# Kernel tuning notes

Hardware: AMD Instinct MI355X
Metric: run time of the kernel (lower is better)

## Reference

```python
import jax, jax.numpy as jnp
import numpy as np

H = 384  # LSTM hidden size


def _conv1d(x, w, b, stride):
    # x: [B, T, Cin], w: [K, Cin, Cout] (flax 'SAME' padding, channels-last)
    y = jax.lax.conv_general_dilated(
        x, w, window_strides=(stride,), padding='SAME',
        dimension_numbers=('NWC', 'WIO', 'NWC'))
    return y + b


def _lstm(x, Wi, Wh, b, reverse):
    # x: [B, T, D]; Wi: [D, 4H] (input proj, no bias in flax LSTMCell input dense),
    # Wh: [H, 4H] (recurrent proj), b: [4H]. Gate order: i, f, g, o.
    if reverse:
        x = x[:, ::-1]
    B = x.shape[0]
    # precompute all input-to-gate projections in one big GEMM: [B, T, 4H]
    xg = jnp.einsum('btd,dh->bth', x, Wi)

    def step(carry, xg_t):
        c, h = carry
        z = xg_t + h @ Wh + b                      # [B, 4H]
        i, f, g, o = jnp.split(z, 4, axis=-1)
        i = jax.nn.sigmoid(i)
        f = jax.nn.sigmoid(f)
        g = jnp.tanh(g)
        o = jax.nn.sigmoid(o)
        c = f * c + i * g
        h = o * jnp.tanh(c)
        return (c, h), h

    init = (jnp.zeros((B, H), x.dtype), jnp.zeros((B, H), x.dtype))
    _, hs = jax.lax.scan(step, init, jnp.swapaxes(xg, 0, 1))  # hs: [T, B, H]
    hs = jnp.swapaxes(hs, 0, 1)
    if reverse:  # keep_order=True: flip output back to original time order
        hs = hs[:, ::-1]
    return hs


def setup_inputs() -> dict:
    key = jax.random.key(0)
    ks = jax.random.split(key, 12)
    s = 0.05
    B, T = 128, 8000
    return {
        'x': jax.random.normal(ks[0], (B, T, 1), jnp.float32),
        'conv1_w': jax.random.normal(ks[1], (5, 1, 4), jnp.float32) * s,
        'conv1_b': jnp.zeros((4,), jnp.float32),
        'conv2_w': jax.random.normal(ks[2], (5, 4, 16), jnp.float32) * s,
        'conv2_b': jnp.zeros((16,), jnp.float32),
        'conv3_w': jax.random.normal(ks[3], (19, 16, H), jnp.float32) * s,
        'conv3_b': jnp.zeros((H,), jnp.float32),
        'lstm_Wi': jax.random.normal(ks[4], (5, H, 4 * H), jnp.float32) * s,
        'lstm_Wh': jax.random.normal(ks[5], (5, H, 4 * H), jnp.float32) * s,
        'lstm_b': jnp.zeros((5, 4 * H), jnp.float32),
        'dense_w': jax.random.normal(ks[6], (H, 5), jnp.float32) * s,
        'dense_b': jnp.zeros((5,), jnp.float32),
    }


def reference(x, conv1_w, conv1_b, conv2_w, conv2_b, conv3_w, conv3_b,
              lstm_Wi, lstm_Wh, lstm_b, dense_w, dense_b):
    # CNN feature extractor
    x = jax.nn.silu(_conv1d(x, conv1_w, conv1_b, 1))
    x = jax.nn.silu(_conv1d(x, conv2_w, conv2_b, 1))
    x = jax.nn.silu(_conv1d(x, conv3_w, conv3_b, 5))   # [B, T/5, 384]
    # 5 stacked LSTMs, layers 1,3,5 reversed (keep_order), layers 2,4 forward
    for i in range(5):
        x = _lstm(x, lstm_Wi[i], lstm_Wh[i], lstm_b[i], reverse=(i % 2 == 0))
    # CTC head
    return x @ dense_w + dense_b                       # [B, T/5, 5]
```

## Files before the change

kernel.cpp:

```cpp
#include <hip/hip_runtime.h>
#include <math.h>

#define B_SZ 128
#define T_IN 8000
#define T_OUT 1600
#define HDIM 384
#define GDIM 1536
#define TC 40
#define NCHUNK (T_OUT / TC)
#define NTILES (12 * (B_SZ * TC / 128))
#define NLB 64

typedef _Float16 f16;
typedef __attribute__((ext_vector_type(2))) _Float16 f16x2;
typedef __attribute__((ext_vector_type(4))) _Float16 f16x4;
typedef __attribute__((ext_vector_type(8))) _Float16 f16x8;
typedef __attribute__((ext_vector_type(4))) float f32x4;
typedef __attribute__((ext_vector_type(4))) unsigned int u32x4;

__device__ inline float fdot2(f16x2 a, f16x2 b, float c) {
#if __has_builtin(__builtin_amdgcn_fdot2)
  return __builtin_amdgcn_fdot2(a, b, c, false);
#else
  return fmaf((float)a[0], (float)b[0], fmaf((float)a[1], (float)b[1], c));
#endif
}

__device__ inline float rcp_fast(float x) {
#if __has_builtin(__builtin_amdgcn_rcpf)
  return __builtin_amdgcn_rcpf(x);
#else
  return 1.f / x;
#endif
}
__device__ inline float sigf(float z) { return rcp_fast(1.f + __expf(-z)); }
__device__ inline float tanh_fast(float z) {
  z = fminf(fmaxf(z, -15.f), 15.f);
  float e = __expf(2.f * z);
  return (e - 1.f) * rcp_fast(e + 1.f);
}

__global__ __launch_bounds__(256) void conv12_kernel(
    const float* __restrict__ x, const float* __restrict__ w1, const float* __restrict__ b1,
    const float* __restrict__ w2, const float* __restrict__ b2, f16* __restrict__ y2) {
  __shared__ float sw1[20], sb1[4], sw2[320], sb2[16];
  int tid = threadIdx.x;
  if (tid < 20) sw1[tid] = w1[tid];
  if (tid < 4)  sb1[tid] = b1[tid];
  if (tid < 16) sb2[tid] = b2[tid];
  for (int i = tid; i < 320; i += 256) sw2[i] = w2[i];
  __syncthreads();
  int flat = blockIdx.x * 256 + tid;
  int b = flat / T_IN, t = flat % T_IN;
  const float* xb = x + (size_t)b * T_IN;
  float xv[9];
#pragma unroll
  for (int d = 0; d < 9; ++d) {
    int tt = t + d - 4;
    xv[d] = (tt >= 0 && tt < T_IN) ? xb[tt] : 0.f;
  }
  float y1[5][4];
#pragma unroll
  for (int u = 0; u < 5; ++u) {
    int tau = t + u - 2;
    bool valid = (tau >= 0 && tau < T_IN);
#pragma unroll
    for (int co = 0; co < 4; ++co) {
      float a = sb1[co];
#pragma unroll
      for (int k = 0; k < 5; ++k) a = fmaf(xv[u + k], sw1[k * 4 + co], a);
      y1[u][co] = valid ? (a / (1.f + expf(-a))) : 0.f;
    }
  }
  f16x8 o0, o1;
#pragma unroll
  for (int co = 0; co < 16; ++co) {
    float a = sb2[co];
#pragma unroll
    for (int u = 0; u < 5; ++u)
#pragma unroll
      for (int ci = 0; ci < 4; ++ci)
        a = fmaf(y1[u][ci], sw2[(u * 4 + ci) * 16 + co], a);
    float sv = a / (1.f + expf(-a));
    if (co < 8) o0[co] = (f16)sv; else o1[co - 8] = (f16)sv;
  }
  f16x8* dst = (f16x8*)(y2 + (size_t)flat * 16);
  dst[0] = o0;
  dst[1] = o1;
}

__global__ __launch_bounds__(256) void w3cvt_kernel(
    const float* __restrict__ w3, f16* __restrict__ w3t) {
  int idx = blockIdx.x * 256 + threadIdx.x;
  int c = idx / 320, k = idx - c * 320;
  w3t[idx] = (k < 304) ? (f16)w3[(size_t)k * 384 + c] : (f16)0.f;
}

#define C3M 32
#define C3K 320
#define INSP 24
#define BSTP 40

__global__ __launch_bounds__(384) void conv3_kernel(
    const f16* __restrict__ y2, const f16* __restrict__ w3t,
    const float* __restrict__ b3, f16* __restrict__ act) {
  __shared__ f16 in_s[176 * INSP];
  __shared__ f16 bs_t[384 * BSTP];
  int tid = threadIdx.x;
  int b = blockIdx.y;
  int t0 = blockIdx.x * C3M;
  int base_t = t0 * 5 - 7;
  for (int j = tid; j < 352; j += 384) {
    int tau = j >> 1, ci0 = (j & 1) * 8;
    int tt = base_t + tau;
    f16x8 v = {};
    if (tt >= 0 && tt < T_IN)
      v = *(const f16x8*)(y2 + ((size_t)b * T_IN + tt) * 16 + ci0);
    *(f16x8*)&in_s[tau * INSP + ci0] = v;
  }
  int wv = tid >> 6;
  int l = tid & 63;
  int lm = l & 15;
  int lk = l >> 4;
  f32x4 acc[2][4];
#pragma unroll
  for (int mt = 0; mt < 2; ++mt)
#pragma unroll
    for (int q = 0; q < 4; ++q) acc[mt][q] = (f32x4){0.f, 0.f, 0.f, 0.f};
  for (int ks = 0; ks < 10; ++ks) {
    __syncthreads();
    for (int u = tid; u < 1536; u += 384) {
      int c = u >> 2, k8 = u & 3;
      *(f16x8*)&bs_t[c * BSTP + k8 * 8] =
          *(const f16x8*)(w3t + (size_t)c * C3K + ks * 32 + k8 * 8);
    }
    __syncthreads();
    int kg = ks * 32 + lk * 8;
    int kk = kg >> 4, ci = kg & 15;
    f16x8 a0 = *(const f16x8*)&in_s[(lm * 5 + kk) * INSP + ci];
    f16x8 a1 = *(const f16x8*)&in_s[((lm + 16) * 5 + kk) * INSP + ci];
#pragma unroll
    for (int q = 0; q < 4; ++q) {
      f16x8 bf = *(const f16x8*)&bs_t[((wv * 4 + q) * 16 + lm) * BSTP + lk * 8];
      acc[0][q] = __builtin_amdgcn_mfma_f32_16x16x32_f16(a0, bf, acc[0][q], 0, 0, 0);
      acc[1][q] = __builtin_amdgcn_mfma_f32_16x16x32_f16(a1, bf, acc[1][q], 0, 0, 0);
    }
  }
#pragma unroll
  for (int mt = 0; mt < 2; ++mt)
#pragma unroll
    for (int q = 0; q < 4; ++q) {
      int n = (wv * 4 + q) * 16 + lm;
      float bv = b3[n];
#pragma unroll
      for (int r = 0; r < 4; ++r) {
        int m = mt * 16 + lk * 4 + r;
        float a = acc[mt][q][r] + bv;
        a = a / (1.f + expf(-a));
        act[((size_t)b * T_OUT + t0 + m) * HDIM + n] = (f16)a;
      }
    }
}

__global__ __launch_bounds__(256) void whcvt_kernel(
    const float* __restrict__ Wh, f16x2* __restrict__ whB) {
  size_t idx = (size_t)blockIdx.x * 256 + threadIdx.x;
  int d = (int)(idx & 3);
  size_t r1 = idx >> 2;
  int lane = (int)(r1 & 63);
  size_t r2 = r1 >> 6;
  int ks = (int)(r2 % 12);
  size_t r3 = r2 / 12;
  int nt = (int)(r3 % 12);
  size_t r4 = r3 / 12;
  int isl = (int)(r4 & 7);
  int L = (int)(r4 >> 3);
  int cz = nt * 16 + (lane & 15);
  int gate = cz & 3;
  int jj = cz >> 2;
  int gcol = gate * 384 + isl * 48 + jj;
  int k2d = ks * 16 + (lane >> 4) * 4 + d;
  const float* src = Wh + ((size_t)L * 384 + 2 * k2d) * 1536 + gcol;
  f16x2 v;
  v[0] = (f16)src[0];
  v[1] = (f16)src[1536];
  whB[idx] = v;
}

__global__ __launch_bounds__(256) void gemm_xg_kernel(
    const f16* __restrict__ act, const float* __restrict__ Bw,
    f16* __restrict__ C, int lo) {
  __shared__ f16x2 As2[8 * 136];
  __shared__ f16x2 Bs2[8 * 128];
  int tid = threadIdx.x;
  int n0 = blockIdx.x * 128;
  int m0 = blockIdx.y * 128;
  int am = tid >> 2;
  int ak = (tid & 3) * 4;
  int bk = tid >> 5;
  int bn = (tid & 31) * 4;
  int row0 = m0 + am, row1 = row0 + 64;
  const f16* Ap0 = act + ((size_t)(row0 / TC) * T_OUT + lo + row0 % TC) * HDIM + ak;
  const f16* Ap1 = act + ((size_t)(row1 / TC) * T_OUT + lo + row1 % TC) * HDIM + ak;
  const float* Bp = Bw + (size_t)(2 * bk) * GDIM + n0 + bn;
  f16x4 ra0 = *(const f16x4*)Ap0;
  f16x4 ra1 = *(const f16x4*)Ap1;
  float4 rb0 = *(const float4*)Bp;
  float4 rb1 = *(const float4*)(Bp + (size_t)GDIM);
  float acc[8][8];
#pragma unroll
  for (int i = 0; i < 8; ++i)
#pragma unroll
    for (int j = 0; j < 8; ++j) acc[i][j] = 0.f;
  int tx = tid & 15, ty = tid >> 4;
  for (int kt = 0; kt < 24; ++kt) {
    int ak2 = ak >> 1;
    As2[(ak2 + 0) * 136 + am] = (f16x2){ra0[0], ra0[1]};
    As2[(ak2 + 1) * 136 + am] = (f16x2){ra0[2], ra0[3]};
    As2[(ak2 + 0) * 136 + am + 64] = (f16x2){ra1[0], ra1[1]};
    As2[(ak2 + 1) * 136 + am + 64] = (f16x2){ra1[2], ra1[3]};
    Bs2[bk * 128 + bn + 0] = (f16x2){(f16)rb0.x, (f16)rb1.x};
    Bs2[bk * 128 + bn + 1] = (f16x2){(f16)rb0.y, (f16)rb1.y};
    Bs2[bk * 128 + bn + 2] = (f16x2){(f16)rb0.z, (f16)rb1.z};
    Bs2[bk * 128 + bn + 3] = (f16x2){(f16)rb0.w, (f16)rb1.w};
    __syncthreads();
    if (kt < 23) {
      Ap0 += 16; Ap1 += 16; Bp += (size_t)16 * GDIM;
      ra0 = *(const f16x4*)Ap0;
      ra1 = *(const f16x4*)Ap1;
      rb0 = *(const float4*)Bp;
      rb1 = *(const float4*)(Bp + (size_t)GDIM);
    }
#pragma unroll
    for (int k2 = 0; k2 < 8; ++k2) {
      f16x8 a0 = *(const f16x8*)&As2[k2 * 136 + ty * 4];
      f16x8 a1 = *(const f16x8*)&As2[k2 * 136 + 64 + ty * 4];
      f16x8 b0 = *(const f16x8*)&Bs2[k2 * 128 + tx * 4];
      f16x8 b1 = *(const f16x8*)&Bs2[k2 * 128 + 64 + tx * 4];
      f16x2 av[8], bv[8];
#pragma unroll
      for (int q = 0; q < 4; ++q) {
        av[q] = (f16x2){a0[2 * q], a0[2 * q + 1]};
        av[q + 4] = (f16x2){a1[2 * q], a1[2 * q + 1]};
        bv[q] = (f16x2){b0[2 * q], b0[2 * q + 1]};
        bv[q + 4] = (f16x2){b1[2 * q], b1[2 * q + 1]};
      }
#pragma unroll
      for (int i = 0; i < 8; ++i)
#pragma unroll
        for (int j = 0; j < 8; ++j) acc[i][j] = fdot2(av[i], bv[j], acc[i][j]);
    }
    __syncthreads();
  }
#pragma unroll
  for (int i = 0; i < 8; ++i) {
    int mi = (i < 4) ? (ty * 4 + i) : (64 + ty * 4 + i - 4);
    f16* Cp = C + (size_t)(m0 + mi) * GDIM + n0;
    f16x4 p0, p1;
    p0[0] = (f16)acc[i][0]; p0[1] = (f16)acc[i][1]; p0[2] = (f16)acc[i][2]; p0[3] = (f16)acc[i][3];
    p1[0] = (f16)acc[i][4]; p1[1] = (f16)acc[i][5]; p1[2] = (f16)acc[i][6]; p1[3] = (f16)acc[i][7];
    *(f16x4*)(Cp + tx * 4) = p0;
    *(f16x4*)(Cp + 64 + tx * 4) = p1;
  }
}

#define HSTR 784

union FusedSh {
  struct { char h2s[16 * HSTR]; unsigned pub[16 * 25]; } L;
  struct { f16x2 As2[3][8 * 136]; f16x2 Bs2[3][8 * 128]; } G;
  char pad[25600];
};

__global__ __launch_bounds__(768, 1) void fused_kernel(
    const f16* __restrict__ xgc_rd, f16* __restrict__ xgc_wr,
    const f16* __restrict__ whB, const float* __restrict__ bias,
    f16* __restrict__ act, float* __restrict__ cst, const float* __restrict__ Wi,
    unsigned* __restrict__ xh,
    int lo_l, int lo_g, int reverse, int first, int do_gemm, int epoch) {
  __shared__ FusedSh sh;
  int tid = threadIdx.x;

  if (blockIdx.x < NLB) {
    int wid = blockIdx.x;
    int g = wid & 7;
    int isl = wid >> 3;
    int b0 = g * 16;
    int nt = tid >> 6;
    int l = tid & 63;
    int bg = l >> 4;
    int qj = (l >> 2) & 3;
    int gate = l & 3;
    int jj = nt * 4 + qj;
    int hcol = isl * 48 + jj;
    int gcol = gate * 384 + isl * 48 + jj;

    f16x8 wreg[12];
    {
      const f16x8* wp = (const f16x8*)whB + (size_t)(isl * 12 + nt) * 12 * 64 + l;
#pragma unroll
      for (int ks = 0; ks < 12; ++ks) wreg[ks] = wp[(size_t)ks * 64];
#pragma unroll
      for (int ks = 0; ks < 12; ++ks) asm volatile("" : "+v"(wreg[ks]));
    }
    float bias_own = bias[gcol];

    float c_reg[4];
    if (first) {
#pragma unroll
      for (int r = 0; r < 4; ++r) c_reg[r] = 0.f;
      for (int i = tid; i < 16 * HSTR / 16; i += 768)
        *(f16x8*)(sh.L.h2s + i * 16) = (f16x8){};
    } else {
      int tprev = reverse ? (lo_l + TC) : (lo_l - 1);
#pragma unroll
      for (int r = 0; r < 4; ++r)
        c_reg[r] = cst[(size_t)(b0 + bg * 4 + r) * HDIM + hcol];
      int flat = tid * 8;
      int bt = flat / 384, c0 = flat % 384;
      *(f16x8*)(sh.L.h2s + bt * HSTR + c0 * 2) =
          *(const f16x8*)(act + ((size_t)(b0 + bt) * T_OUT + tprev) * HDIM + c0);
    }
    __syncthreads();

    const char* arow = sh.L.h2s + (l & 15) * HSTR + (l >> 4) * 16;
    unsigned short* pubh = (unsigned short*)sh.L.pub;

    int k2 = (tid % 3 == 0) ? (768 + tid / 3) : -1;

    float xv[4];
    {
      int tl0 = reverse ? (TC - 1) : 0;
      const f16* xb = xgc_rd + ((size_t)(b0 + bg * 4) * TC + tl0) * GDIM + gcol;
#pragma unroll
      for (int r = 0; r < 4; ++r) xv[r] = (float)xb[(size_t)r * TC * GDIM];
    }

    for (int s = 0; s < TC; ++s) {
      int t = reverse ? (lo_l + TC - 1 - s) : (lo_l + s);

      f32x4 acc = {0.f, 0.f, 0.f, 0.f};
#pragma unroll
      for (int ks = 0; ks < 12; ++ks) {
        f16x8 a = *(const f16x8*)(arow + ks * 64);
        acc = __builtin_amdgcn_mfma_f32_16x16x32_f16(a, wreg[ks], acc, 0, 0, 0);
      }

      f16 h16[4];
#pragma unroll
      for (int r = 0; r < 4; ++r) {
        float a = acc[r] + xv[r] + bias_own;
        float b = __shfl_xor(a, 1);
        float cc = __shfl_xor(a, 2);
        float dd = __shfl_xor(b, 2);
        float zi = (gate == 0) ? a : (gate == 1) ? b : (gate == 2) ? cc : dd;
        float zf = (gate == 1) ? a : (gate == 0) ? b : (gate == 3) ? cc : dd;
        float zg = (gate == 2) ? a : (gate == 3) ? b : (gate == 0) ? cc : dd;
        float zo = (gate == 3) ? a : (gate == 2) ? b : (gate == 1) ? cc : dd;
        float ig = sigf(zi), fg = sigf(zf), gv = tanh_fast(zg), og = sigf(zo);
        c_reg[r] = fg * c_reg[r] + ig * gv;
        h16[r] = (f16)(og * tanh_fast(c_reg[r]));
      }

      if (s + 1 < TC) {
        unsigned tag = (unsigned)(epoch * TC + s + 1);
        unsigned* slotbase = xh + (size_t)(s & 1) * 128 * 256;

        if (gate == 0) {
          int lcol = nt * 4 + qj;
#pragma unroll
          for (int r = 0; r < 4; ++r)
            pubh[(bg * 4 + r) * 50 + lcol] = __builtin_bit_cast(unsigned short, h16[r]);
        }
        __syncthreads();

        if (tid < 128) {
          int bt = tid >> 3, u = tid & 7;
          const unsigned* pw = sh.L.pub + bt * 25 + u * 3;
          u32x4 dnew;
          dnew[0] = pw[0]; dnew[1] = pw[1]; dnew[2] = pw[2]; dnew[3] = tag;
          u32x4* dp = (u32x4*)(slotbase + (((size_t)(b0 + bt) * 64) + isl * 8 + u) * 4);
          asm volatile("global_store_dwordx4 %0, %1, off sc0 sc1"
                       :: "v"(dp), "v"(dnew) : "memory");
        }

        if (gate == 0) {
#pragma unroll
          for (int r = 0; r < 4; ++r)
            act[((size_t)(b0 + bg * 4 + r) * T_OUT + t) * HDIM + hcol] = h16[r];
        }
        {
          int tl_n = reverse ? (TC - 2 - s) : (s + 1);
          const f16* xb = xgc_rd + ((size_t)(b0 + bg * 4) * TC + tl_n) * GDIM + gcol;
#pragma unroll
          for (int r = 0; r < 4; ++r) xv[r] = (float)xb[(size_t)r * TC * GDIM];
        }

        const u32x4* upA = nullptr; const u32x4* upB = nullptr;
        unsigned* dstA = nullptr; unsigned* dstB = nullptr;
#pragma unroll
        for (int uu = 0; uu < 2; ++uu) {
          int k = (uu == 0) ? tid : k2;
          if (uu == 1 && k < 0) break;
          int bt = k >> 6, rem = k & 63;
          int isl_src = rem >> 3, u = rem & 7;
          unsigned* dst = (unsigned*)(sh.L.h2s + bt * HSTR + isl_src * 96 + u * 12);
          if (isl_src == isl) {
            const unsigned* pw = sh.L.pub + bt * 25 + u * 3;
            dst[0] = pw[0]; dst[1] = pw[1]; dst[2] = pw[2];
          } else {
            const u32x4* up = (const u32x4*)(slotbase + (((size_t)(b0 + bt) * 64) + rem) * 4);
            if (!upA) { upA = up; dstA = dst; } else { upB = up; dstB = dst; }
          }
        }
        if (upA && !upB) {
          u32x4 v;
          while (true) {
            asm volatile("global_load_dwordx4 %0, %1, off sc0 sc1\n\ts_waitcnt vmcnt(0)"
                         : "=v"(v) : "v"(upA) : "memory");
            if (v[3] >= tag) break;
            __builtin_amdgcn_s_sleep(1);
          }
          dstA[0] = v[0]; dstA[1] = v[1]; dstA[2] = v[2];
        } else if (upA && upB) {
          u32x4 v0, v1;
          while (true) {
            asm volatile("global_load_dwordx4 %0, %2, off sc0 sc1\n\t"
                         "global_load_dwordx4 %1, %3, off sc0 sc1\n\t"
                         "s_waitcnt vmcnt(0)"
                         : "=&v"(v0), "=&v"(v1) : "v"(upA), "v"(upB) : "memory");
            if (v0[3] >= tag && v1[3] >= tag) break;
            __builtin_amdgcn_s_sleep(1);
          }
          dstA[0] = v0[0]; dstA[1] = v0[1]; dstA[2] = v0[2];
          dstB[0] = v1[0]; dstB[1] = v1[1]; dstB[2] = v1[2];
        }
        __syncthreads();
      } else {
        if (gate == 0) {
#pragma unroll
          for (int r = 0; r < 4; ++r)
            act[((size_t)(b0 + bg * 4 + r) * T_OUT + t) * HDIM + hcol] = h16[r];
        }
      }
    }
    if (gate == 0) {
#pragma unroll
      for (int r = 0; r < 4; ++r)
        cst[(size_t)(b0 + bg * 4 + r) * HDIM + hcol] = c_reg[r];
    }
  } else {
    if (!do_gemm) return;
    int wid = blockIdx.x - NLB;
    int sub = tid >> 8;
    int stid = tid & 255;
    int tileid = wid + 192 * sub;
    bool valid = (tileid < NTILES);
    int tclamp = valid ? tileid : 0;
    int n0 = (tclamp % 12) * 128;
    int m0 = (tclamp / 12) * 128;
    f16x2* As2 = &sh.G.As2[sub][0];
    f16x2* Bs2 = &sh.G.Bs2[sub][0];
    int am = stid >> 2;
    int ak = (stid & 3) * 4;
    int bk = stid >> 5;
    int bn = (stid & 31) * 4;
    int row0 = m0 + am, row1 = row0 + 64;
    const f16* Ap0 = act + ((size_t)(row0 / TC) * T_OUT + lo_g + row0 % TC) * HDIM + ak;
    const f16* Ap1 = act + ((size_t)(row1 / TC) * T_OUT + lo_g + row1 % TC) * HDIM + ak;
    const float* Bp = Wi + (size_t)(2 * bk) * GDIM + n0 + bn;
    f16x4 ra0 = {}, ra1 = {};
    float4 rb0 = {}, rb1 = {};
    if (valid) {
      ra0 = *(const f16x4*)Ap0;
      ra1 = *(const f16x4*)Ap1;
      rb0 = *(const float4*)Bp;
      rb1 = *(const float4*)(Bp + (size_t)GDIM);
    }
    float acc[8][8];
#pragma unroll
    for (int i = 0; i < 8; ++i)
#pragma unroll
      for (int j = 0; j < 8; ++j) acc[i][j] = 0.f;
    int tx = stid & 15, ty = stid >> 4;
    for (int kt = 0; kt < 24; ++kt) {
      if (valid) {
        int ak2 = ak >> 1;
        As2[(ak2 + 0) * 136 + am] = (f16x2){ra0[0], ra0[1]};
        As2[(ak2 + 1) * 136 + am] = (f16x2){ra0[2], ra0[3]};
        As2[(ak2 + 0) * 136 + am + 64] = (f16x2){ra1[0], ra1[1]};
        As2[(ak2 + 1) * 136 + am + 64] = (f16x2){ra1[2], ra1[3]};
        Bs2[bk * 128 + bn + 0] = (f16x2){(f16)rb0.x, (f16)rb1.x};
        Bs2[bk * 128 + bn + 1] = (f16x2){(f16)rb0.y, (f16)rb1.y};
        Bs2[bk * 128 + bn + 2] = (f16x2){(f16)rb0.z, (f16)rb1.z};
        Bs2[bk * 128 + bn + 3] = (f16x2){(f16)rb0.w, (f16)rb1.w};
      }
      __syncthreads();
      if (valid) {
        if (kt < 23) {
          Ap0 += 16; Ap1 += 16; Bp += (size_t)16 * GDIM;
          ra0 = *(const f16x4*)Ap0;
          ra1 = *(const f16x4*)Ap1;
          rb0 = *(const float4*)Bp;
          rb1 = *(const float4*)(Bp + (size_t)GDIM);
        }
#pragma unroll
        for (int k2i = 0; k2i < 8; ++k2i) {
          f16x8 a0 = *(const f16x8*)&As2[k2i * 136 + ty * 4];
          f16x8 a1 = *(const f16x8*)&As2[k2i * 136 + 64 + ty * 4];
          f16x8 b0 = *(const f16x8*)&Bs2[k2i * 128 + tx * 4];
          f16x8 b1 = *(const f16x8*)&Bs2[k2i * 128 + 64 + tx * 4];
          f16x2 av[8], bv[8];
#pragma unroll
          for (int qq = 0; qq < 4; ++qq) {
            av[qq] = (f16x2){a0[2 * qq], a0[2 * qq + 1]};
            av[qq + 4] = (f16x2){a1[2 * qq], a1[2 * qq + 1]};
            bv[qq] = (f16x2){b0[2 * qq], b0[2 * qq + 1]};
            bv[qq + 4] = (f16x2){b1[2 * qq], b1[2 * qq + 1]};
          }
#pragma unroll
          for (int i = 0; i < 8; ++i)
#pragma unroll
            for (int j = 0; j < 8; ++j) acc[i][j] = fdot2(av[i], bv[j], acc[i][j]);
        }
      }
      __syncthreads();
    }
    if (valid) {
#pragma unroll
      for (int i = 0; i < 8; ++i) {
        int mi = (i < 4) ? (ty * 4 + i) : (64 + ty * 4 + i - 4);
        f16* Cp = xgc_wr + (size_t)(m0 + mi) * GDIM + n0;
        f16x4 p0, p1;
        p0[0] = (f16)acc[i][0]; p0[1] = (f16)acc[i][1]; p0[2] = (f16)acc[i][2]; p0[3] = (f16)acc[i][3];
        p1[0] = (f16)acc[i][4]; p1[1] = (f16)acc[i][5]; p1[2] = (f16)acc[i][6]; p1[3] = (f16)acc[i][7];
        *(f16x4*)(Cp + tx * 4) = p0;
        *(f16x4*)(Cp + 64 + tx * 4) = p1;
      }
    }
  }
}

__global__ __launch_bounds__(256) void dense_kernel(
    const f16* __restrict__ h, const float* __restrict__ dw,
    const float* __restrict__ db, float* __restrict__ out) {
  __shared__ float ws_[1920];
  __shared__ float bs[5];
  int tid = threadIdx.x;
  for (int i = tid; i < 1920; i += 256) ws_[i] = dw[i];
  if (tid < 5) bs[tid] = db[tid];
  __syncthreads();
  size_t flat = (size_t)blockIdx.x * 256 + tid;
  const f16* hp = h + flat * HDIM;
  float acc[5];
#pragma unroll
  for (int o = 0; o < 5; ++o) acc[o] = bs[o];
  for (int d = 0; d < HDIM; d += 4) {
    f16x4 hv = *(const f16x4*)(hp + d);
#pragma unroll
    for (int o = 0; o < 5; ++o) {
      acc[o] = fmaf((float)hv[0], ws_[(d + 0) * 5 + o], acc[o]);
      acc[o] = fmaf((float)hv[1], ws_[(d + 1) * 5 + o], acc[o]);
      acc[o] = fmaf((float)hv[2], ws_[(d + 2) * 5 + o], acc[o]);
      acc[o] = fmaf((float)hv[3], ws_[(d + 3) * 5 + o], acc[o]);
    }
  }
  float* op = out + flat * 5;
#pragma unroll
  for (int o = 0; o < 5; ++o) op[o] = acc[o];
}

extern "C" void kernel_launch(void* const* d_in, const int* in_sizes, int n_in,
                              void* d_out, int out_size, void* d_ws, size_t ws_size,
                              hipStream_t stream) {
  const float* x  = (const float*)d_in[0];
  const float* w1 = (const float*)d_in[1];
  const float* b1 = (const float*)d_in[2];
  const float* w2 = (const float*)d_in[3];
  const float* b2 = (const float*)d_in[4];
  const float* w3 = (const float*)d_in[5];
  const float* b3 = (const float*)d_in[6];
  const float* Wi = (const float*)d_in[7];
  const float* Wh = (const float*)d_in[8];
  const float* lb = (const float*)d_in[9];
  const float* dw = (const float*)d_in[10];
  const float* db = (const float*)d_in[11];
  float* out = (float*)d_out;
  char* ws = (char*)d_ws;

  const size_t ACT_BYTES = (size_t)B_SZ * T_OUT * HDIM * 2;
  const size_t XGC_BYTES = (size_t)B_SZ * TC * GDIM * 2;
  const size_t WHB_BYTES = (size_t)5 * 8 * 12 * 12 * 64 * 16;
  const size_t CST_BYTES = (size_t)B_SZ * HDIM * 4;
  const size_t XH_BYTES  = (size_t)2 * 128 * 64 * 16;
  const size_t W3T_BYTES = (size_t)384 * 320 * 2;
  f16*      act  = (f16*)ws;
  f16*      xgcA = (f16*)(ws + ACT_BYTES);
  f16*      xgcB = (f16*)(ws + ACT_BYTES + XGC_BYTES);
  f16*      whB  = (f16*)(ws + ACT_BYTES + 2 * XGC_BYTES);
  float*    cst  = (float*)(ws + ACT_BYTES + 2 * XGC_BYTES + WHB_BYTES);
  unsigned* xh   = (unsigned*)(ws + ACT_BYTES + 2 * XGC_BYTES + WHB_BYTES + CST_BYTES);
  f16*      w3t  = (f16*)(ws + ACT_BYTES + 2 * XGC_BYTES + WHB_BYTES + CST_BYTES + XH_BYTES);
  f16* y2 = xgcA;

  hipMemsetAsync(xh, 0, XH_BYTES, stream);

  hipLaunchKernelGGL(conv12_kernel, dim3(B_SZ * T_IN / 256), dim3(256), 0, stream,
                     x, w1, b1, w2, b2, y2);
  hipLaunchKernelGGL(w3cvt_kernel, dim3(384 * 320 / 256), dim3(256), 0, stream,
                     w3, w3t);
  hipLaunchKernelGGL(conv3_kernel, dim3(T_OUT / C3M, B_SZ), dim3(384), 0, stream,
                     y2, w3t, b3, act);
  hipLaunchKernelGGL(whcvt_kernel, dim3((unsigned)(WHB_BYTES / 4 / 256)), dim3(256), 0, stream,
                     Wh, (f16x2*)whB);

  for (int l = 0; l < 5; ++l) {
    int rev = (l % 2 == 0) ? 1 : 0;
    const float* wi_p = Wi + (size_t)l * HDIM * GDIM;
    const f16* wh_p = whB + (size_t)l * 8 * 12 * 12 * 64 * 8;
    const float* lb_p = lb + (size_t)l * GDIM;
    int lo0 = rev ? (T_OUT - TC) : 0;
    hipLaunchKernelGGL(gemm_xg_kernel, dim3(GDIM / 128, (B_SZ * TC) / 128), dim3(256), 0, stream,
                       act, wi_p, xgcA, lo0);
    for (int ci = 0; ci < NCHUNK; ++ci) {
      int lo_l = rev ? (T_OUT - (ci + 1) * TC) : (ci * TC);
      int do_gemm = (ci + 1 < NCHUNK) ? 1 : 0;
      int lo_g = do_gemm ? (rev ? (T_OUT - (ci + 2) * TC) : ((ci + 1) * TC)) : 0;
      f16* rd = (ci % 2 == 0) ? xgcA : xgcB;
      f16* wr = (ci % 2 == 0) ? xgcB : xgcA;
      int epoch = l * NCHUNK + ci;
      hipLaunchKernelGGL(fused_kernel, dim3(256), dim3(768), 0, stream,
                         rd, wr, wh_p, lb_p, act, cst, wi_p, xh,
                         lo_l, lo_g, rev, (ci == 0) ? 1 : 0, do_gemm, epoch);
    }
  }
  hipLaunchKernelGGL(dense_kernel, dim3((B_SZ * T_OUT) / 256), dim3(256), 0, stream,
                     act, dw, db, out);
}
```

Baseline: 26.47 ms.

## Make each LSTM layer one persistent kernel with counter-based GEMM/recurrence pipelining

Each layer previously used one projection GEMM launch plus 40 fused chunk launches. Now a single persistent launch per layer loops over all chunks. The recurrence blocks and the input-projection GEMM blocks hand off through global atomic counters, so the GEMM can run ahead into the double buffer while the recurrence consumes. The cell state stays in registers across chunks, which removes the save/restore through global memory and the per-launch overhead. In exchange this depends on all 256 blocks being co-resident, and it adds spin-wait and cache-bypassing loads and stores.

```diff
diff --git a/kernel.cpp b/kernel.cpp
--- a/kernel.cpp
+++ b/kernel.cpp
@@ -17,6 +17,7 @@
 typedef __attribute__((ext_vector_type(8))) _Float16 f16x8;
 typedef __attribute__((ext_vector_type(4))) float f32x4;
 typedef __attribute__((ext_vector_type(4))) unsigned int u32x4;
+typedef __attribute__((ext_vector_type(2))) unsigned int u32x2;
 
 __device__ inline float fdot2(f16x2 a, f16x2 b, float c) {
 #if __has_builtin(__builtin_amdgcn_fdot2)
@@ -38,6 +39,10 @@
   z = fminf(fmaxf(z, -15.f), 15.f);
   float e = __expf(2.f * z);
   return (e - 1.f) * rcp_fast(e + 1.f);
+}
+__device__ inline float u16f(unsigned u) {
+  unsigned short us = (unsigned short)u;
+  return (float)__builtin_bit_cast(_Float16, us);
 }
 
 __global__ __launch_bounds__(256) void conv12_kernel(
@@ -187,83 +192,6 @@
   whB[idx] = v;
 }
 
-__global__ __launch_bounds__(256) void gemm_xg_kernel(
-    const f16* __restrict__ act, const float* __restrict__ Bw,
-    f16* __restrict__ C, int lo) {
-  __shared__ f16x2 As2[8 * 136];
-  __shared__ f16x2 Bs2[8 * 128];
-  int tid = threadIdx.x;
-  int n0 = blockIdx.x * 128;
-  int m0 = blockIdx.y * 128;
-  int am = tid >> 2;
-  int ak = (tid & 3) * 4;
-  int bk = tid >> 5;
-  int bn = (tid & 31) * 4;
-  int row0 = m0 + am, row1 = row0 + 64;
-  const f16* Ap0 = act + ((size_t)(row0 / TC) * T_OUT + lo + row0 % TC) * HDIM + ak;
-  const f16* Ap1 = act + ((size_t)(row1 / TC) * T_OUT + lo + row1 % TC) * HDIM + ak;
-  const float* Bp = Bw + (size_t)(2 * bk) * GDIM + n0 + bn;
-  f16x4 ra0 = *(const f16x4*)Ap0;
-  f16x4 ra1 = *(const f16x4*)Ap1;
-  float4 rb0 = *(const float4*)Bp;
-  float4 rb1 = *(const float4*)(Bp + (size_t)GDIM);
-  float acc[8][8];
-#pragma unroll
-  for (int i = 0; i < 8; ++i)
-#pragma unroll
-    for (int j = 0; j < 8; ++j) acc[i][j] = 0.f;
-  int tx = tid & 15, ty = tid >> 4;
-  for (int kt = 0; kt < 24; ++kt) {
-    int ak2 = ak >> 1;
-    As2[(ak2 + 0) * 136 + am] = (f16x2){ra0[0], ra0[1]};
-    As2[(ak2 + 1) * 136 + am] = (f16x2){ra0[2], ra0[3]};
-    As2[(ak2 + 0) * 136 + am + 64] = (f16x2){ra1[0], ra1[1]};
-    As2[(ak2 + 1) * 136 + am + 64] = (f16x2){ra1[2], ra1[3]};
-    Bs2[bk * 128 + bn + 0] = (f16x2){(f16)rb0.x, (f16)rb1.x};
-    Bs2[bk * 128 + bn + 1] = (f16x2){(f16)rb0.y, (f16)rb1.y};
-    Bs2[bk * 128 + bn + 2] = (f16x2){(f16)rb0.z, (f16)rb1.z};
-    Bs2[bk * 128 + bn + 3] = (f16x2){(f16)rb0.w, (f16)rb1.w};
-    __syncthreads();
-    if (kt < 23) {
-      Ap0 += 16; Ap1 += 16; Bp += (size_t)16 * GDIM;
-      ra0 = *(const f16x4*)Ap0;
-      ra1 = *(const f16x4*)Ap1;
-      rb0 = *(const float4*)Bp;
-      rb1 = *(const float4*)(Bp + (size_t)GDIM);
-    }
-#pragma unroll
-    for (int k2 = 0; k2 < 8; ++k2) {
-      f16x8 a0 = *(const f16x8*)&As2[k2 * 136 + ty * 4];
-      f16x8 a1 = *(const f16x8*)&As2[k2 * 136 + 64 + ty * 4];
-      f16x8 b0 = *(const f16x8*)&Bs2[k2 * 128 + tx * 4];
-      f16x8 b1 = *(const f16x8*)&Bs2[k2 * 128 + 64 + tx * 4];
-      f16x2 av[8], bv[8];
-#pragma unroll
-      for (int q = 0; q < 4; ++q) {
-        av[q] = (f16x2){a0[2 * q], a0[2 * q + 1]};
-        av[q + 4] = (f16x2){a1[2 * q], a1[2 * q + 1]};
-        bv[q] = (f16x2){b0[2 * q], b0[2 * q + 1]};
-        bv[q + 4] = (f16x2){b1[2 * q], b1[2 * q + 1]};
-      }
-#pragma unroll
-      for (int i = 0; i < 8; ++i)
-#pragma unroll
-        for (int j = 0; j < 8; ++j) acc[i][j] = fdot2(av[i], bv[j], acc[i][j]);
-    }
-    __syncthreads();
-  }
-#pragma unroll
-  for (int i = 0; i < 8; ++i) {
-    int mi = (i < 4) ? (ty * 4 + i) : (64 + ty * 4 + i - 4);
-    f16* Cp = C + (size_t)(m0 + mi) * GDIM + n0;
-    f16x4 p0, p1;
-    p0[0] = (f16)acc[i][0]; p0[1] = (f16)acc[i][1]; p0[2] = (f16)acc[i][2]; p0[3] = (f16)acc[i][3];
-    p1[0] = (f16)acc[i][4]; p1[1] = (f16)acc[i][5]; p1[2] = (f16)acc[i][6]; p1[3] = (f16)acc[i][7];
-    *(f16x4*)(Cp + tx * 4) = p0;
-    *(f16x4*)(Cp + 64 + tx * 4) = p1;
-  }
-}
-
 #define HSTR 784
 
 union FusedSh {
@@ -272,12 +200,12 @@
   char pad[25600];
 };
 
-__global__ __launch_bounds__(768, 1) void fused_kernel(
-    const f16* __restrict__ xgc_rd, f16* __restrict__ xgc_wr,
+__global__ __launch_bounds__(768, 1) void fused_layer_kernel(
+    f16* __restrict__ xgA, f16* __restrict__ xgB,
     const f16* __restrict__ whB, const float* __restrict__ bias,
-    f16* __restrict__ act, float* __restrict__ cst, const float* __restrict__ Wi,
-    unsigned* __restrict__ xh,
-    int lo_l, int lo_g, int reverse, int first, int do_gemm, int epoch) {
+    f16* __restrict__ act, const float* __restrict__ Wi,
+    unsigned* __restrict__ xh, unsigned* __restrict__ ctr2,
+    int rev, int gbase) {
   __shared__ FusedSh sh;
   int tid = threadIdx.x;
 
@@ -287,17 +215,17 @@
     int isl = wid >> 3;
     int b0 = g * 16;
     int nt = tid >> 6;
-    int l = tid & 63;
-    int bg = l >> 4;
-    int qj = (l >> 2) & 3;
-    int gate = l & 3;
+    int ln = tid & 63;
+    int bg = ln >> 4;
+    int qj = (ln >> 2) & 3;
+    int gate = ln & 3;
     int jj = nt * 4 + qj;
     int hcol = isl * 48 + jj;
     int gcol = gate * 384 + isl * 48 + jj;
 
     f16x8 wreg[12];
     {
-      const f16x8* wp = (const f16x8*)whB + (size_t)(isl * 12 + nt) * 12 * 64 + l;
+      const f16x8* wp = (const f16x8*)whB + (size_t)(isl * 12 + nt) * 12 * 64 + ln;
 #pragma unroll
       for (int ks = 0; ks < 12; ++ks) wreg[ks] = wp[(size_t)ks * 64];
 #pragma unroll
@@ -306,151 +234,156 @@
     float bias_own = bias[gcol];
 
     float c_reg[4];
-    if (first) {
-#pragma unroll
-      for (int r = 0; r < 4; ++r) c_reg[r] = 0.f;
-      for (int i = tid; i < 16 * HSTR / 16; i += 768)
-        *(f16x8*)(sh.L.h2s + i * 16) = (f16x8){};
-    } else {
-      int tprev = reverse ? (lo_l + TC) : (lo_l - 1);
-#pragma unroll
-      for (int r = 0; r < 4; ++r)
-        c_reg[r] = cst[(size_t)(b0 + bg * 4 + r) * HDIM + hcol];
-      int flat = tid * 8;
-      int bt = flat / 384, c0 = flat % 384;
-      *(f16x8*)(sh.L.h2s + bt * HSTR + c0 * 2) =
-          *(const f16x8*)(act + ((size_t)(b0 + bt) * T_OUT + tprev) * HDIM + c0);
-    }
+#pragma unroll
+    for (int r = 0; r < 4; ++r) c_reg[r] = 0.f;
+    for (int i = tid; i < 16 * HSTR / 16; i += 768)
+      *(f16x8*)(sh.L.h2s + i * 16) = (f16x8){};
     __syncthreads();
 
-    const char* arow = sh.L.h2s + (l & 15) * HSTR + (l >> 4) * 16;
+    const char* arow = sh.L.h2s + (ln & 15) * HSTR + (ln >> 4) * 16;
     unsigned short* pubh = (unsigned short*)sh.L.pub;
-
     int k2 = (tid % 3 == 0) ? (768 + tid / 3) : -1;
 
-    float xv[4];
-    {
-      int tl0 = reverse ? (TC - 1) : 0;
-      const f16* xb = xgc_rd + ((size_t)(b0 + bg * 4) * TC + tl0) * GDIM + gcol;
-#pragma unroll
-      for (int r = 0; r < 4; ++r) xv[r] = (float)xb[(size_t)r * TC * GDIM];
-    }
-
-    for (int s = 0; s < TC; ++s) {
-      int t = reverse ? (lo_l + TC - 1 - s) : (lo_l + s);
-
-      f32x4 acc = {0.f, 0.f, 0.f, 0.f};
-#pragma unroll
-      for (int ks = 0; ks < 12; ++ks) {
-        f16x8 a = *(const f16x8*)(arow + ks * 64);
-        acc = __builtin_amdgcn_mfma_f32_16x16x32_f16(a, wreg[ks], acc, 0, 0, 0);
-      }
-
-      f16 h16[4];
-#pragma unroll
-      for (int r = 0; r < 4; ++r) {
-        float a = acc[r] + xv[r] + bias_own;
-        float b = __shfl_xor(a, 1);
-        float cc = __shfl_xor(a, 2);
-        float dd = __shfl_xor(b, 2);
-        float zi = (gate == 0) ? a : (gate == 1) ? b : (gate == 2) ? cc : dd;
-        float zf = (gate == 1) ? a : (gate == 0) ? b : (gate == 3) ? cc : dd;
-        float zg = (gate == 2) ? a : (gate == 3) ? b : (gate == 0) ? cc : dd;
-        float zo = (gate == 3) ? a : (gate == 2) ? b : (gate == 1) ? cc : dd;
-        float ig = sigf(zi), fg = sigf(zf), gv = tanh_fast(zg), og = sigf(zo);
-        c_reg[r] = fg * c_reg[r] + ig * gv;
-        h16[r] = (f16)(og * tanh_fast(c_reg[r]));
-      }
-
-      if (s + 1 < TC) {
-        unsigned tag = (unsigned)(epoch * TC + s + 1);
-        unsigned* slotbase = xh + (size_t)(s & 1) * 128 * 256;
-
-        if (gate == 0) {
-          int lcol = nt * 4 + qj;
-#pragma unroll
-          for (int r = 0; r < 4; ++r)
-            pubh[(bg * 4 + r) * 50 + lcol] = __builtin_bit_cast(unsigned short, h16[r]);
+    for (int ci = 0; ci < NCHUNK; ++ci) {
+      int gci = gbase + ci;
+      if (tid == 0) {
+        unsigned tgt = 192u * (unsigned)(ci + 1);
+        while (__hip_atomic_load(&ctr2[1], __ATOMIC_RELAXED, __HIP_MEMORY_SCOPE_AGENT) < tgt)
+          __builtin_amdgcn_s_sleep(2);
+      }
+      __syncthreads();
+      const f16* xgc_rd = (ci & 1) ? xgB : xgA;
+      int lo_l = rev ? (T_OUT - (ci + 1) * TC) : (ci * TC);
+
+      unsigned xr[4];
+      {
+        int tl0 = rev ? (TC - 1) : 0;
+        const f16* xb = xgc_rd + ((size_t)(b0 + bg * 4) * TC + tl0) * GDIM + gcol;
+#pragma unroll
+        for (int r = 0; r < 4; ++r)
+          asm volatile("global_load_ushort %0, %1, off sc0 sc1"
+                       : "=v"(xr[r]) : "v"(xb + (size_t)r * TC * GDIM) : "memory");
+        asm volatile("s_waitcnt vmcnt(0)" ::: "memory");
+        __builtin_amdgcn_sched_barrier(0);
+      }
+
+      for (int s = 0; s < TC; ++s) {
+        int t = rev ? (lo_l + TC - 1 - s) : (lo_l + s);
+
+        f32x4 acc = {0.f, 0.f, 0.f, 0.f};
+#pragma unroll
+        for (int ks = 0; ks < 12; ++ks) {
+          f16x8 a = *(const f16x8*)(arow + ks * 64);
+          acc = __builtin_amdgcn_mfma_f32_16x16x32_f16(a, wreg[ks], acc, 0, 0, 0);
         }
-        __syncthreads();
-
-        if (tid < 128) {
-          int bt = tid >> 3, u = tid & 7;
-          const unsigned* pw = sh.L.pub + bt * 25 + u * 3;
-          u32x4 dnew;
-          dnew[0] = pw[0]; dnew[1] = pw[1]; dnew[2] = pw[2]; dnew[3] = tag;
-          u32x4* dp = (u32x4*)(slotbase + (((size_t)(b0 + bt) * 64) + isl * 8 + u) * 4);
-          asm volatile("global_store_dwordx4 %0, %1, off sc0 sc1"
-                       :: "v"(dp), "v"(dnew) : "memory");
+
+        f16 h16[4];
+#pragma unroll
+        for (int r = 0; r < 4; ++r) {
+          float a = acc[r] + u16f(xr[r]) + bias_own;
+          float b = __shfl_xor(a, 1);
+          float cc = __shfl_xor(a, 2);
+          float dd = __shfl_xor(b, 2);
+          float zi = (gate == 0) ? a : (gate == 1) ? b : (gate == 2) ? cc : dd;
+          float zf = (gate == 1) ? a : (gate == 0) ? b : (gate == 3) ? cc : dd;
+          float zg = (gate == 2) ? a : (gate == 3) ? b : (gate == 0) ? cc : dd;
+          float zo = (gate == 3) ? a : (gate == 2) ? b : (gate == 1) ? cc : dd;
+          float ig = sigf(zi), fg = sigf(zf), gv = tanh_fast(zg), og = sigf(zo);
+          c_reg[r] = fg * c_reg[r] + ig * gv;
+          h16[r] = (f16)(og * tanh_fast(c_reg[r]));
         }
 
-        if (gate == 0) {
-#pragma unroll
-          for (int r = 0; r < 4; ++r)
-            act[((size_t)(b0 + bg * 4 + r) * T_OUT + t) * HDIM + hcol] = h16[r];
+        bool exch = (s + 1 < TC) || (ci + 1 < NCHUNK);
+        if (exch) {
+          unsigned tag = (unsigned)(gci * TC + s + 1);
+          unsigned* slotbase = xh + (size_t)(s & 1) * 128 * 256;
+
+          if (gate == 0) {
+            int lcol = nt * 4 + qj;
+#pragma unroll
+            for (int r = 0; r < 4; ++r)
+              pubh[(bg * 4 + r) * 50 + lcol] = __builtin_bit_cast(unsigned short, h16[r]);
+          }
+          __syncthreads();
+
+          if (tid < 128) {
+            int bt = tid >> 3, u = tid & 7;
+            const unsigned* pw = sh.L.pub + bt * 25 + u * 3;
+            u32x4 dnew;
+            dnew[0] = pw[0]; dnew[1] = pw[1]; dnew[2] = pw[2]; dnew[3] = tag;
+            u32x4* dp = (u32x4*)(slotbase + (((size_t)(b0 + bt) * 64) + isl * 8 + u) * 4);
+            asm volatile("global_store_dwordx4 %0, %1, off sc0 sc1"
+                         :: "v"(dp), "v"(dnew) : "memory");
+          }
+
+          if (gate == 0) {
+#pragma unroll
+            for (int r = 0; r < 4; ++r)
+              act[((size_t)(b0 + bg * 4 + r) * T_OUT + t) * HDIM + hcol] = h16[r];
+          }
+          if (s + 1 < TC) {
+            int tl_n = rev ? (TC - 2 - s) : (s + 1);
+            const f16* xb = xgc_rd + ((size_t)(b0 + bg * 4) * TC + tl_n) * GDIM + gcol;
+#pragma unroll
+            for (int r = 0; r < 4; ++r)
+              asm volatile("global_load_ushort %0, %1, off sc0 sc1"
+                           : "=v"(xr[r]) : "v"(xb + (size_t)r * TC * GDIM) : "memory");
+          }
+
+          const u32x4* upA = nullptr; const u32x4* upB = nullptr;
+          unsigned* dstA = nullptr; unsigned* dstB = nullptr;
+#pragma unroll
+          for (int uu = 0; uu < 2; ++uu) {
+            int k = (uu == 0) ? tid : k2;
+            if (uu == 1 && k < 0) break;
+            int bt = k >> 6, rem = k & 63;
+            int isl_src = rem >> 3, u = rem & 7;
+            unsigned* dst = (unsigned*)(sh.L.h2s + bt * HSTR + isl_src * 96 + u * 12);
+            if (isl_src == isl) {
+              const unsigned* pw = sh.L.pub + bt * 25 + u * 3;
+              dst[0] = pw[0]; dst[1] = pw[1]; dst[2] = pw[2];
+            } else {
+              const u32x4* up = (const u32x4*)(slotbase + (((size_t)(b0 + bt) * 64) + rem) * 4);
+              if (!upA) { upA = up; dstA = dst; } else { upB = up; dstB = dst; }
+            }
+          }
+          if (upA && !upB) {
+            u32x4 v;
+            while (true) {
+              asm volatile("global_load_dwordx4 %0, %1, off sc0 sc1\n\ts_waitcnt vmcnt(0)"
+                           : "=v"(v) : "v"(upA) : "memory");
+              if (v[3] >= tag) break;
+              __builtin_amdgcn_s_sleep(1);
+            }
+            dstA[0] = v[0]; dstA[1] = v[1]; dstA[2] = v[2];
+          } else if (upA && upB) {
+            u32x4 v0, v1;
+            while (true) {
+              asm volatile("global_load_dwordx4 %0, %2, off sc0 sc1\n\t"
+                           "global_load_dwordx4 %1, %3, off sc0 sc1\n\t"
+                           "s_waitcnt vmcnt(0)"
+                           : "=&v"(v0), "=&v"(v1) : "v"(upA), "v"(upB) : "memory");
+              if (v0[3] >= tag && v1[3] >= tag) break;
+              __builtin_amdgcn_s_sleep(1);
+            }
+            dstA[0] = v0[0]; dstA[1] = v0[1]; dstA[2] = v0[2];
+            dstB[0] = v1[0]; dstB[1] = v1[1]; dstB[2] = v1[2];
+          }
+          asm volatile("s_waitcnt vmcnt(0)" ::: "memory");
+          __builtin_amdgcn_sched_barrier(0);
+          __syncthreads();
+        } else {
+          if (gate == 0) {
+#pragma unroll
+            for (int r = 0; r < 4; ++r)
+              act[((size_t)(b0 + bg * 4 + r) * T_OUT + t) * HDIM + hcol] = h16[r];
+          }
         }
-        {
-          int tl_n = reverse ? (TC - 2 - s) : (s + 1);
-          const f16* xb = xgc_rd + ((size_t)(b0 + bg * 4) * TC + tl_n) * GDIM + gcol;
-#pragma unroll
-          for (int r = 0; r < 4; ++r) xv[r] = (float)xb[(size_t)r * TC * GDIM];
-        }
-
-        const u32x4* upA = nullptr; const u32x4* upB = nullptr;
-        unsigned* dstA = nullptr; unsigned* dstB = nullptr;
-#pragma unroll
-        for (int uu = 0; uu < 2; ++uu) {
-          int k = (uu == 0) ? tid : k2;
-          if (uu == 1 && k < 0) break;
-          int bt = k >> 6, rem = k & 63;
-          int isl_src = rem >> 3, u = rem & 7;
-          unsigned* dst = (unsigned*)(sh.L.h2s + bt * HSTR + isl_src * 96 + u * 12);
-          if (isl_src == isl) {
-            const unsigned* pw = sh.L.pub + bt * 25 + u * 3;
-            dst[0] = pw[0]; dst[1] = pw[1]; dst[2] = pw[2];
-          } else {
-            const u32x4* up = (const u32x4*)(slotbase + (((size_t)(b0 + bt) * 64) + rem) * 4);
-            if (!upA) { upA = up; dstA = dst; } else { upB = up; dstB = dst; }
-          }
-        }
-        if (upA && !upB) {
-          u32x4 v;
-          while (true) {
-            asm volatile("global_load_dwordx4 %0, %1, off sc0 sc1\n\ts_waitcnt vmcnt(0)"
-                         : "=v"(v) : "v"(upA) : "memory");
-            if (v[3] >= tag) break;
-            __builtin_amdgcn_s_sleep(1);
-          }
-          dstA[0] = v[0]; dstA[1] = v[1]; dstA[2] = v[2];
-        } else if (upA && upB) {
-          u32x4 v0, v1;
-          while (true) {
-            asm volatile("global_load_dwordx4 %0, %2, off sc0 sc1\n\t"
-                         "global_load_dwordx4 %1, %3, off sc0 sc1\n\t"
-                         "s_waitcnt vmcnt(0)"
-                         : "=&v"(v0), "=&v"(v1) : "v"(upA), "v"(upB) : "memory");
-            if (v0[3] >= tag && v1[3] >= tag) break;
-            __builtin_amdgcn_s_sleep(1);
-          }
-          dstA[0] = v0[0]; dstA[1] = v0[1]; dstA[2] = v0[2];
-          dstB[0] = v1[0]; dstB[1] = v1[1]; dstB[2] = v1[2];
-        }
-        __syncthreads();
-      } else {
-        if (gate == 0) {
-#pragma unroll
-          for (int r = 0; r < 4; ++r)
-            act[((size_t)(b0 + bg * 4 + r) * T_OUT + t) * HDIM + hcol] = h16[r];
-        }
-      }
-    }
-    if (gate == 0) {
-#pragma unroll
-      for (int r = 0; r < 4; ++r)
-        cst[(size_t)(b0 + bg * 4 + r) * HDIM + hcol] = c_reg[r];
+      }
+      if (tid == 0)
+        __hip_atomic_fetch_add(&ctr2[0], 1u, __ATOMIC_RELAXED, __HIP_MEMORY_SCOPE_AGENT);
     }
   } else {
-    if (!do_gemm) return;
     int wid = blockIdx.x - NLB;
     int sub = tid >> 8;
     int stid = tid & 255;
@@ -465,78 +398,97 @@
     int ak = (stid & 3) * 4;
     int bk = stid >> 5;
     int bn = (stid & 31) * 4;
+    int tx = stid & 15, ty = stid >> 4;
     int row0 = m0 + am, row1 = row0 + 64;
-    const f16* Ap0 = act + ((size_t)(row0 / TC) * T_OUT + lo_g + row0 % TC) * HDIM + ak;
-    const f16* Ap1 = act + ((size_t)(row1 / TC) * T_OUT + lo_g + row1 % TC) * HDIM + ak;
-    const float* Bp = Wi + (size_t)(2 * bk) * GDIM + n0 + bn;
-    f16x4 ra0 = {}, ra1 = {};
-    float4 rb0 = {}, rb1 = {};
-    if (valid) {
-      ra0 = *(const f16x4*)Ap0;
-      ra1 = *(const f16x4*)Ap1;
-      rb0 = *(const float4*)Bp;
-      rb1 = *(const float4*)(Bp + (size_t)GDIM);
-    }
-    float acc[8][8];
-#pragma unroll
-    for (int i = 0; i < 8; ++i)
-#pragma unroll
-      for (int j = 0; j < 8; ++j) acc[i][j] = 0.f;
-    int tx = stid & 15, ty = stid >> 4;
-    for (int kt = 0; kt < 24; ++kt) {
+
+    for (int ci = 0; ci < NCHUNK; ++ci) {
+      if (ci >= 2 && tid == 0) {
+        unsigned tgt = 64u * (unsigned)(ci - 1);
+        while (__hip_atomic_load(&ctr2[0], __ATOMIC_RELAXED, __HIP_MEMORY_SCOPE_AGENT) < tgt)
+          __builtin_amdgcn_s_sleep(2);
+      }
+      __syncthreads();
+      int lo = rev ? (T_OUT - (ci + 1) * TC) : (ci * TC);
+      f16* Cbuf = (ci & 1) ? xgB : xgA;
+      const f16* Ap0 = act + ((size_t)(row0 / TC) * T_OUT + lo + row0 % TC) * HDIM + ak;
+      const f16* Ap1 = act + ((size_t)(row1 / TC) * T_OUT + lo + row1 % TC) * HDIM + ak;
+      const float* Bp = Wi + (size_t)(2 * bk) * GDIM + n0 + bn;
+      f16x4 ra0 = {}, ra1 = {};
+      float4 rb0 = {}, rb1 = {};
       if (valid) {
-        int ak2 = ak >> 1;
-        As2[(ak2 + 0) * 136 + am] = (f16x2){ra0[0], ra0[1]};
-        As2[(ak2 + 1) * 136 + am] = (f16x2){ra0[2], ra0[3]};
-        As2[(ak2 + 0) * 136 + am + 64] = (f16x2){ra1[0], ra1[1]};
-        As2[(ak2 + 1) * 136 + am + 64] = (f16x2){ra1[2], ra1[3]};
-        Bs2[bk * 128 + bn + 0] = (f16x2){(f16)rb0.x, (f16)rb1.x};
-        Bs2[bk * 128 + bn + 1] = (f16x2){(f16)rb0.y, (f16)rb1.y};
-        Bs2[bk * 128 + bn + 2] = (f16x2){(f16)rb0.z, (f16)rb1.z};
-        Bs2[bk * 128 + bn + 3] = (f16x2){(f16)rb0.w, (f16)rb1.w};
-      }
+        ra0 = *(const f16x4*)Ap0;
+        ra1 = *(const f16x4*)Ap1;
+        rb0 = *(const float4*)Bp;
+        rb1 = *(const float4*)(Bp + (size_t)GDIM);
+      }
+      float acc[8][8];
+#pragma unroll
+      for (int i = 0; i < 8; ++i)
+#pragma unroll
+        for (int j = 0; j < 8; ++j) acc[i][j] = 0.f;
+      for (int kt = 0; kt < 24; ++kt) {
+        if (valid) {
+          int ak2 = ak >> 1;
+          As2[(ak2 + 0) * 136 + am] = (f16x2){ra0[0], ra0[1]};
+          As2[(ak2 + 1) * 136 + am] = (f16x2){ra0[2], ra0[3]};
+          As2[(ak2 + 0) * 136 + am + 64] = (f16x2){ra1[0], ra1[1]};
+          As2[(ak2 + 1) * 136 + am + 64] = (f16x2){ra1[2], ra1[3]};
+          Bs2[bk * 128 + bn + 0] = (f16x2){(f16)rb0.x, (f16)rb1.x};
+          Bs2[bk * 128 + bn + 1] = (f16x2){(f16)rb0.y, (f16)rb1.y};
+          Bs2[bk * 128 + bn + 2] = (f16x2){(f16)rb0.z, (f16)rb1.z};
+          Bs2[bk * 128 + bn + 3] = (f16x2){(f16)rb0.w, (f16)rb1.w};
+        }
+        __syncthreads();
+        if (valid) {
+          if (kt < 23) {
+            Ap0 += 16; Ap1 += 16; Bp += (size_t)16 * GDIM;
+            ra0 = *(const f16x4*)Ap0;
+            ra1 = *(const f16x4*)Ap1;
+            rb0 = *(const float4*)Bp;
+            rb1 = *(const float4*)(Bp + (size_t)GDIM);
+          }
+#pragma unroll
+          for (int k2i = 0; k2i < 8; ++k2i) {
+            f16x8 a0 = *(const f16x8*)&As2[k2i * 136 + ty * 4];
+            f16x8 a1 = *(const f16x8*)&As2[k2i * 136 + 64 + ty * 4];
+            f16x8 b0 = *(const f16x8*)&Bs2[k2i * 128 + tx * 4];
+            f16x8 b1 = *(const f16x8*)&Bs2[k2i * 128 + 64 + tx * 4];
+            f16x2 av[8], bv[8];
+#pragma unroll
+            for (int qq = 0; qq < 4; ++qq) {
+              av[qq] = (f16x2){a0[2 * qq], a0[2 * qq + 1]};
+              av[qq + 4] = (f16x2){a1[2 * qq], a1[2 * qq + 1]};
+              bv[qq] = (f16x2){b0[2 * qq], b0[2 * qq + 1]};
+              bv[qq + 4] = (f16x2){b1[2 * qq], b1[2 * qq + 1]};
+            }
+#pragma unroll
+            for (int i = 0; i < 8; ++i)
+#pragma unroll
+              for (int j = 0; j < 8; ++j) acc[i][j] = fdot2(av[i], bv[j], acc[i][j]);
+          }
+        }
+        __syncthreads();
+      }
+      if (valid) {
+#pragma unroll
+        for (int i = 0; i < 8; ++i) {
+          int mi = (i < 4) ? (ty * 4 + i) : (64 + ty * 4 + i - 4);
+          f16* Cp = Cbuf + (size_t)(m0 + mi) * GDIM + n0;
+          f16x4 p0, p1;
+          p0[0] = (f16)acc[i][0]; p0[1] = (f16)acc[i][1]; p0[2] = (f16)acc[i][2]; p0[3] = (f16)acc[i][3];
+          p1[0] = (f16)acc[i][4]; p1[1] = (f16)acc[i][5]; p1[2] = (f16)acc[i][6]; p1[3] = (f16)acc[i][7];
+          u32x2 q0 = __builtin_bit_cast(u32x2, p0);
+          u32x2 q1 = __builtin_bit_cast(u32x2, p1);
+          asm volatile("global_store_dwordx2 %0, %2, off sc0 sc1\n\t"
+                       "global_store_dwordx2 %1, %3, off sc0 sc1"
+                       :: "v"(Cp + tx * 4), "v"(Cp + 64 + tx * 4), "v"(q0), "v"(q1)
+                       : "memory");
+        }
+      }
+      asm volatile("s_waitcnt vmcnt(0)" ::: "memory");
       __syncthreads();
-      if (valid) {
-        if (kt < 23) {
-          Ap0 += 16; Ap1 += 16; Bp += (size_t)16 * GDIM;
-          ra0 = *(const f16x4*)Ap0;
-          ra1 = *(const f16x4*)Ap1;
-          rb0 = *(const float4*)Bp;
-          rb1 = *(const float4*)(Bp + (size_t)GDIM);
-        }
-#pragma unroll
-        for (int k2i = 0; k2i < 8; ++k2i) {
-          f16x8 a0 = *(const f16x8*)&As2[k2i * 136 + ty * 4];
-          f16x8 a1 = *(const f16x8*)&As2[k2i * 136 + 64 + ty * 4];
-          f16x8 b0 = *(const f16x8*)&Bs2[k2i * 128 + tx * 4];
-          f16x8 b1 = *(const f16x8*)&Bs2[k2i * 128 + 64 + tx * 4];
-          f16x2 av[8], bv[8];
-#pragma unroll
-          for (int qq = 0; qq < 4; ++qq) {
-            av[qq] = (f16x2){a0[2 * qq], a0[2 * qq + 1]};
-            av[qq + 4] = (f16x2){a1[2 * qq], a1[2 * qq + 1]};
-            bv[qq] = (f16x2){b0[2 * qq], b0[2 * qq + 1]};
-            bv[qq + 4] = (f16x2){b1[2 * qq], b1[2 * qq + 1]};
-          }
-#pragma unroll
-          for (int i = 0; i < 8; ++i)
-#pragma unroll
-            for (int j = 0; j < 8; ++j) acc[i][j] = fdot2(av[i], bv[j], acc[i][j]);
-        }
-      }
-      __syncthreads();
-    }
-    if (valid) {
-#pragma unroll
-      for (int i = 0; i < 8; ++i) {
-        int mi = (i < 4) ? (ty * 4 + i) : (64 + ty * 4 + i - 4);
-        f16* Cp = xgc_wr + (size_t)(m0 + mi) * GDIM + n0;
-        f16x4 p0, p1;
-        p0[0] = (f16)acc[i][0]; p0[1] = (f16)acc[i][1]; p0[2] = (f16)acc[i][2]; p0[3] = (f16)acc[i][3];
-        p1[0] = (f16)acc[i][4]; p1[1] = (f16)acc[i][5]; p1[2] = (f16)acc[i][6]; p1[3] = (f16)acc[i][7];
-        *(f16x4*)(Cp + tx * 4) = p0;
-        *(f16x4*)(Cp + 64 + tx * 4) = p1;
-      }
+      if (tid == 0)
+        __hip_atomic_fetch_add(&ctr2[1], 1u, __ATOMIC_RELAXED, __HIP_MEMORY_SCOPE_AGENT);
     }
   }
 }
@@ -591,19 +543,18 @@
   const size_t ACT_BYTES = (size_t)B_SZ * T_OUT * HDIM * 2;
   const size_t XGC_BYTES = (size_t)B_SZ * TC * GDIM * 2;
   const size_t WHB_BYTES = (size_t)5 * 8 * 12 * 12 * 64 * 16;
-  const size_t CST_BYTES = (size_t)B_SZ * HDIM * 4;
   const size_t XH_BYTES  = (size_t)2 * 128 * 64 * 16;
-  const size_t W3T_BYTES = (size_t)384 * 320 * 2;
+  const size_t CTR_BYTES = 64;
   f16*      act  = (f16*)ws;
   f16*      xgcA = (f16*)(ws + ACT_BYTES);
   f16*      xgcB = (f16*)(ws + ACT_BYTES + XGC_BYTES);
   f16*      whB  = (f16*)(ws + ACT_BYTES + 2 * XGC_BYTES);
-  float*    cst  = (float*)(ws + ACT_BYTES + 2 * XGC_BYTES + WHB_BYTES);
-  unsigned* xh   = (unsigned*)(ws + ACT_BYTES + 2 * XGC_BYTES + WHB_BYTES + CST_BYTES);
-  f16*      w3t  = (f16*)(ws + ACT_BYTES + 2 * XGC_BYTES + WHB_BYTES + CST_BYTES + XH_BYTES);
+  unsigned* xh   = (unsigned*)(ws + ACT_BYTES + 2 * XGC_BYTES + WHB_BYTES);
+  unsigned* ctr  = (unsigned*)(ws + ACT_BYTES + 2 * XGC_BYTES + WHB_BYTES + XH_BYTES);
+  f16*      w3t  = (f16*)(ws + ACT_BYTES + 2 * XGC_BYTES + WHB_BYTES + XH_BYTES + CTR_BYTES);
   f16* y2 = xgcA;
 
-  hipMemsetAsync(xh, 0, XH_BYTES, stream);
+  hipMemsetAsync(xh, 0, XH_BYTES + CTR_BYTES, stream);
 
   hipLaunchKernelGGL(conv12_kernel, dim3(B_SZ * T_IN / 256), dim3(256), 0, stream,
                      x, w1, b1, w2, b2, y2);
@@ -619,20 +570,9 @@
     const float* wi_p = Wi + (size_t)l * HDIM * GDIM;
     const f16* wh_p = whB + (size_t)l * 8 * 12 * 12 * 64 * 8;
     const float* lb_p = lb + (size_t)l * GDIM;
-    int lo0 = rev ? (T_OUT - TC) : 0;
-    hipLaunchKernelGGL(gemm_xg_kernel, dim3(GDIM / 128, (B_SZ * TC) / 128), dim3(256), 0, stream,
-                       act, wi_p, xgcA, lo0);
-    for (int ci = 0; ci < NCHUNK; ++ci) {
-      int lo_l = rev ? (T_OUT - (ci + 1) * TC) : (ci * TC);
-      int do_gemm = (ci + 1 < NCHUNK) ? 1 : 0;
-      int lo_g = do_gemm ? (rev ? (T_OUT - (ci + 2) * TC) : ((ci + 1) * TC)) : 0;
-      f16* rd = (ci % 2 == 0) ? xgcA : xgcB;
-      f16* wr = (ci % 2 == 0) ? xgcB : xgcA;
-      int epoch = l * NCHUNK + ci;
-      hipLaunchKernelGGL(fused_kernel, dim3(256), dim3(768), 0, stream,
-                         rd, wr, wh_p, lb_p, act, cst, wi_p, xh,
-                         lo_l, lo_g, rev, (ci == 0) ? 1 : 0, do_gemm, epoch);
-    }
+    hipLaunchKernelGGL(fused_layer_kernel, dim3(256), dim3(768), 0, stream,
+                       xgcA, xgcB, wh_p, lb_p, act, wi_p, xh, ctr + l * 2,
+                       rev, l * NCHUNK);
   }
   hipLaunchKernelGGL(dense_kernel, dim3((B_SZ * T_OUT) / 256), dim3(256), 0, stream,
                      act, dw, db, out);
```

Measured after the change: 29.12 ms. +10.0%, slower.
